# Performance work log

Hardware: AMD Instinct MI355X
Metric: run time of the kernel (lower is better)

The kernel has to match this reference:

```python
import jax, jax.numpy as jnp
import numpy as np

N, C = 4194304, 10
EPS = 1e-10
FOCAL_EPS = 1e-8
TEMP, THETA = 0.01, 0.1
NUM_TH = 21


def setup_inputs() -> dict:
    key = jax.random.key(0)
    k1, k2 = jax.random.split(key)
    logits = jax.random.normal(k1, (N, C), dtype=jnp.float32)
    probs = jax.nn.softmax(logits, axis=1)
    labels = jax.random.randint(k2, (N,), 0, C)
    y = jax.nn.one_hot(labels, C, dtype=jnp.float32)
    return {"probs": probs, "y": y}


def _soft_T(e):
    # sigmoid( (1/temp) * log( e*(1-theta) / clamp((1-e)*theta, eps) ) )
    num = e * (1.0 - THETA)
    den = jnp.maximum((1.0 - e) * THETA, EPS)
    frac = jnp.maximum(num / den, EPS)
    return jax.nn.sigmoid(jnp.log(frac) / TEMP)


def reference(probs, y):
    entmax = jnp.log(jnp.asarray(C, dtype=probs.dtype))
    predictions = jnp.argmax(probs, axis=1)             # [N]
    labels = jnp.argmax(y)                              # scalar (flattened argmax, as in torch code)

    # predictive uncertainty (type=0): entropy of probs per-sample
    unc = -jnp.sum(probs * jnp.log(jnp.maximum(probs, EPS)), axis=1)  # [N]

    th_list = jnp.linspace(0.0, 1.0, NUM_TH, dtype=probs.dtype)       # [21]
    umin, umax = jnp.min(unc), jnp.max(unc)
    unc_th = umin + th_list * (umax - umin)                           # [21]

    s = _soft_T(unc / entmax)                                         # [N]
    t = jnp.tanh(unc)                                                 # [N]
    w_cert = (1.0 - s) * (1.0 - t)   # weight when counted as 'certain'
    w_unc = s * t                    # weight when counted as 'uncertain'

    acc = (predictions == labels).astype(probs.dtype)                 # [N]
    inacc = 1.0 - acc

    le = (unc[None, :] <= unc_th[:, None]).astype(probs.dtype)        # [21, N]
    gt = 1.0 - le

    # one parallel masked-reduction pass over all 21 thresholds
    n_ac = le @ (acc * w_cert)
    n_au = gt @ (acc * w_unc)
    n_ic = le @ (inacc * w_cert)
    n_iu = gt @ (inacc * w_unc)

    avu = (n_ac + n_iu) / (n_ac + n_au + n_ic + n_iu + EPS)           # [21]

    # trapezoid rule over increasing th_list (direction = +1)
    dx = jnp.diff(th_list)
    auc_avu = jnp.sum((avu[1:] + avu[:-1]) * 0.5 * dx)

    # FocalLoss(gamma=1)
    logp = jnp.log(jnp.maximum(probs, FOCAL_EPS))
    ce_per = -jnp.sum(y * logp, axis=1)
    focal_per = -jnp.sum(y * logp * (1.0 - probs), axis=1)
    focal_loss = jnp.mean(focal_per)
    ce_loss = jnp.mean(ce_per)

    beta = 1.0
    savu_loss = -beta * jnp.log(jnp.maximum(auc_avu, EPS)) + focal_loss
    return (savu_loss, ce_loss)
```

## Files before the change

### kernel.cpp

```cpp
#include <hip/hip_runtime.h>

#define C 10
#define CHUNK_ROWS 128
#define CHUNK_FLOATS 1280

__device__ __forceinline__ float waveSum(float v) {
#pragma unroll
  for (int o = 32; o > 0; o >>= 1) v += __shfl_down(v, o, 64);
  return v;
}
__device__ __forceinline__ float waveMin(float v) {
#pragma unroll
  for (int o = 32; o > 0; o >>= 1) v = fminf(v, __shfl_down(v, o, 64));
  return v;
}
__device__ __forceinline__ float waveMax(float v) {
#pragma unroll
  for (int o = 32; o > 0; o >>= 1) v = fmaxf(v, __shfl_down(v, o, 64));
  return v;
}
__device__ __forceinline__ unsigned waveMaxU(unsigned v) {
#pragma unroll
  for (int o = 32; o > 0; o >>= 1) {
    unsigned w = (unsigned)__shfl_down((int)v, o, 64);
    v = v > w ? v : w;
  }
  return v;
}

#define GLD16(gp, lp)                                             \
  __builtin_amdgcn_global_load_lds(                               \
      (__attribute__((address_space(1))) void*)(gp),              \
      (__attribute__((address_space(3))) void*)(lp), 16, 0, 0)

__global__ __launch_bounds__(128, 2) void pass1(
    const float* __restrict__ probs, const float* __restrict__ y,
    float2* __restrict__ us2,
    unsigned* __restrict__ uminInvSlots, unsigned* __restrict__ umaxSlots,
    float* __restrict__ ceSlots, float* __restrict__ focalSlots,
    int nchunks) {
  __shared__ float lds[2 * 2 * 2 * CHUNK_FLOATS];
  __shared__ float red[8];
  const int tid = threadIdx.x;
  const int widx = tid >> 6, lane = tid & 63;
  float* const wbase = lds + widx * (4 * CHUNK_FLOATS);

  const int gw = blockIdx.x * 2 + widx;
  const int NW = gridDim.x * 2;

  int label0 = 0;
  {
    float m = y[0];
#pragma unroll
    for (int c = 1; c < C; ++c) {
      float v = y[c];
      if (v > m) { m = v; label0 = c; }
    }
  }

  auto issue = [&](int c, int b) {
    const size_t g = (size_t)c * CHUNK_FLOATS + (size_t)lane * 4;
    float* lp = wbase + b * (2 * CHUNK_FLOATS);
#pragma unroll
    for (int q = 0; q < 5; ++q)
      GLD16(probs + g + q * 256, lp + q * 256 + lane * 4);
#pragma unroll
    for (int q = 0; q < 5; ++q)
      GLD16(y + g + q * 256, lp + CHUNK_FLOATS + q * 256 + lane * 4);
  };

  float ceA = 0.f, foA = 0.f;
  float mnA = __uint_as_float(0x7f800000u), mxA = 0.f;

  if (gw < nchunks) issue(gw, 0);
  int b = 0;
  for (int c = gw; c < nchunks; c += NW, b ^= 1) {
    if (c + NW < nchunks) issue(c + NW, b ^ 1);

    const float4* pp = (const float4*)(wbase + b * (2 * CHUNK_FLOATS));
    const float4* yy = (const float4*)(wbase + b * (2 * CHUNK_FLOATS) + CHUNK_FLOATS);
    float P[20], Yv[20];
#pragma unroll
    for (int q = 0; q < 5; ++q) {
      float4 v = pp[lane * 5 + q];
      P[4 * q] = v.x; P[4 * q + 1] = v.y; P[4 * q + 2] = v.z; P[4 * q + 3] = v.w;
    }
#pragma unroll
    for (int q = 0; q < 5; ++q) {
      float4 v = yy[lane * 5 + q];
      Yv[4 * q] = v.x; Yv[4 * q + 1] = v.y; Yv[4 * q + 2] = v.z; Yv[4 * q + 3] = v.w;
    }

    int am0 = 0, am1 = 0;
    float m0 = P[0], m1 = P[10];
#pragma unroll
    for (int cc = 1; cc < C; ++cc) {
      if (P[cc] > m0) { m0 = P[cc]; am0 = cc; }
      if (P[10 + cc] > m1) { m1 = P[10 + cc]; am1 = cc; }
    }
    float u0 = 0.f, u1 = 0.f, pl0 = 0.f, pl1 = 0.f;
#pragma unroll
    for (int cc = 0; cc < C; ++cc) {
      u0 -= P[cc] * __logf(fmaxf(P[cc], 1e-10f));
      u1 -= P[10 + cc] * __logf(fmaxf(P[10 + cc], 1e-10f));
      pl0 = fmaf(Yv[cc], P[cc], pl0);
      pl1 = fmaf(Yv[10 + cc], P[10 + cc], pl1);
    }
    float ce0 = -__logf(fmaxf(pl0, 1e-8f)), ce1 = -__logf(fmaxf(pl1, 1e-8f));
    ceA += ce0 + ce1;
    foA += ce0 * (1.f - pl0) + ce1 * (1.f - pl1);
    mnA = fminf(mnA, fminf(u0, u1));
    mxA = fmaxf(mxA, fmaxf(u0, u1));

    unsigned s0 = __float_as_uint(u0) | ((am0 == label0) ? 0u : 0x80000000u);
    unsigned s1 = __float_as_uint(u1) | ((am1 == label0) ? 0u : 0x80000000u);
    us2[(size_t)c * 64 + lane] = make_float2(__uint_as_float(s0), __uint_as_float(s1));
  }

  float ce = waveSum(ceA), fo = waveSum(foA);
  float mn = waveMin(mnA), mx = waveMax(mxA);
  if (lane == 0) { red[widx] = ce; red[2 + widx] = fo; red[4 + widx] = mn; red[6 + widx] = mx; }
  __syncthreads();
  if (tid == 0) {
    float tce = red[0] + red[1];
    float tfo = red[2] + red[3];
    float tmn = fminf(red[4], red[5]);
    float tmx = fmaxf(red[6], red[7]);
    int slot = blockIdx.x & 63;
    atomicAdd(&ceSlots[slot], tce);
    atomicAdd(&focalSlots[slot], tfo);
    atomicMax(&uminInvSlots[slot], ~__float_as_uint(tmn));
    atomicMax(&umaxSlots[slot], __float_as_uint(tmx));
  }
}

__global__ __launch_bounds__(256, 4) void pass2(
    const float4* __restrict__ us4, int n4,
    const unsigned* __restrict__ uminInvSlots, const unsigned* __restrict__ umaxSlots,
    float* __restrict__ ghist) {
  __shared__ float hist[88 * 64];
  __shared__ float smm[2];
  const int tid = threadIdx.x, lane = tid & 63;
  for (int i = tid; i < 88 * 64; i += 256) hist[i] = 0.f;
  if (tid < 64) {
    unsigned mnInv = waveMaxU(uminInvSlots[tid]);
    unsigned mxb = waveMaxU(umaxSlots[tid]);
    if (tid == 0) { smm[0] = __uint_as_float(~mnInv); smm[1] = __uint_as_float(mxb); }
  }
  __syncthreads();
  const float umin = smm[0], delta = smm[1] - smm[0];
  float th[21];
#pragma unroll
  for (int k = 0; k < 21; ++k) th[k] = fmaf(0.05f * (float)k, delta, umin);

  const int stride = gridDim.x * 256;
  for (int i = blockIdx.x * 256 + tid; i < n4; i += stride) {
    float4 v = us4[i];
    float vv[4] = {v.x, v.y, v.z, v.w};
#pragma unroll
    for (int q = 0; q < 4; ++q) {
      unsigned b = __float_as_uint(vv[q]);
      int rb = (b >> 31) ? 44 : 0;
      float u = __uint_as_float(b & 0x7fffffffu);
      float e = u * 0.4342944819f;
      float lnum = __logf(e * 0.9f);
      float lden = __logf(fmaxf((1.f - e) * 0.1f, 1e-10f));
      float x = fmaxf(lnum - lden, -23.0258509f) * 100.f;
      float s = __builtin_amdgcn_rcpf(1.f + __expf(-x));
      float t = 1.f - 2.f * __builtin_amdgcn_rcpf(__expf(2.f * u) + 1.f);
      float wc = (1.f - s) * (1.f - t), wu = s * t;
      int j = 0;
#pragma unroll
      for (int k = 0; k < 21; ++k) j += (u > th[k]) ? 1 : 0;
      atomicAdd(&hist[(rb + j) * 64 + lane], wc);
      atomicAdd(&hist[(rb + 22 + j) * 64 + lane], wu);
    }
  }
  __syncthreads();
#pragma unroll
  for (int st = 32; st >= 1; st >>= 1) {
    for (int idx = tid; idx < 88 * st; idx += 256) {
      int r = idx / st, c = idx - r * st;
      hist[r * 64 + c] += hist[r * 64 + c + st];
    }
    __syncthreads();
  }
  int slot = blockIdx.x & 63;
  for (int r = tid; r < 88; r += 256)
    atomicAdd(&ghist[slot * 88 + r], hist[r * 64]);
}

__global__ __launch_bounds__(256) void pass3(
    const float* __restrict__ ghist,
    const float* __restrict__ ceSlots, const float* __restrict__ focalSlots,
    float* __restrict__ out, float invN) {
  __shared__ float hr[88];
  __shared__ float scf[2];
  int tid = threadIdx.x;
  if (tid < 88) {
    float s = 0.f;
    for (int q = 0; q < 64; ++q) s += ghist[q * 88 + tid];
    hr[tid] = s;
  }
  if (tid >= 128 && tid < 192) {
    int l = tid - 128;
    float ce = waveSum(ceSlots[l]);
    float fo = waveSum(focalSlots[l]);
    if (l == 0) { scf[0] = ce; scf[1] = fo; }
  }
  __syncthreads();
  if (tid == 0) {
    float H0[22], H1[22], H2[22], H3[22];
    float totAU = 0.f, totIU = 0.f;
    for (int j = 0; j < 22; ++j) {
      H0[j] = hr[j]; H1[j] = hr[22 + j]; H2[j] = hr[44 + j]; H3[j] = hr[66 + j];
      totAU += H1[j]; totIU += H3[j];
    }
    float n_ac = 0.f, n_ic = 0.f, n_au = totAU, n_iu = totIU;
    float auc = 0.f, prev = 0.f;
    for (int k = 0; k < 21; ++k) {
      n_ac += H0[k]; n_ic += H2[k];
      n_au -= H1[k]; n_iu -= H3[k];
      float avu = (n_ac + n_iu) / (n_ac + n_au + n_ic + n_iu + 1e-10f);
      if (k > 0) auc += (avu + prev) * 0.5f * 0.05f;
      prev = avu;
    }
    out[0] = -logf(fmaxf(auc, 1e-10f)) + scf[1] * invN;
    out[1] = scf[0] * invN;
  }
}

extern "C" void kernel_launch(void* const* d_in, const int* in_sizes, int n_in,
                              void* d_out, int out_size, void* d_ws, size_t ws_size,
                              hipStream_t stream) {
  const float* probs = (const float*)d_in[0];
  const float* y = (const float*)d_in[1];
  float* out = (float*)d_out;
  const int N = in_sizes[0] / C;

  float* wsf = (float*)d_ws;
  unsigned* uminInvSlots = (unsigned*)wsf;
  unsigned* umaxSlots = (unsigned*)(wsf + 64);
  float* ceSlots = wsf + 128;
  float* focalSlots = wsf + 192;
  float* ghist = wsf + 256;
  float* us = wsf + 5888;

  hipMemsetAsync(d_ws, 0, 5888 * sizeof(float), stream);

  const int nchunks = N / CHUNK_ROWS;
  pass1<<<1024, 128, 0, stream>>>(probs, y, (float2*)us, uminInvSlots, umaxSlots,
                                  ceSlots, focalSlots, nchunks);
  pass2<<<1024, 256, 0, stream>>>((const float4*)us, N / 4, uminInvSlots, umaxSlots,
                                  ghist);
  pass3<<<1, 256, 0, stream>>>(ghist, ceSlots, focalSlots, out, 1.0f / (float)N);
}
```

Baseline: 406.4 us.

## Load y directly to registers, compute focal terms per-element, widen pass1 blocks

The one-hot y tensor is now prefetched straight into registers in a coalesced layout instead of being staged through LDS, which halves LDS use per wave. The cross-entropy and focal terms are computed elementwise, as sum(y*log p) and sum(y*log p*(1-p)), instead of via the gathered label probability. Blocks grow to 4 waves, so the grid has twice as many waves, and the per-block shared reduction is replaced by per-wave atomics. This costs more log evaluations per element, more registers for the double-buffered y values, and more atomics.

After: 399.9 us. No clear change (-1.6%).

```diff
diff --git a/kernel.cpp b/kernel.cpp
--- a/kernel.cpp
+++ b/kernel.cpp
@@ -33,20 +33,19 @@
       (__attribute__((address_space(1))) void*)(gp),              \
       (__attribute__((address_space(3))) void*)(lp), 16, 0, 0)
 
-__global__ __launch_bounds__(128, 2) void pass1(
+__global__ __launch_bounds__(256, 4) void pass1(
     const float* __restrict__ probs, const float* __restrict__ y,
     float2* __restrict__ us2,
     unsigned* __restrict__ uminInvSlots, unsigned* __restrict__ umaxSlots,
     float* __restrict__ ceSlots, float* __restrict__ focalSlots,
     int nchunks) {
-  __shared__ float lds[2 * 2 * 2 * CHUNK_FLOATS];
-  __shared__ float red[8];
+  __shared__ float lds[4 * 2 * CHUNK_FLOATS];
   const int tid = threadIdx.x;
   const int widx = tid >> 6, lane = tid & 63;
-  float* const wbase = lds + widx * (4 * CHUNK_FLOATS);
-
-  const int gw = blockIdx.x * 2 + widx;
-  const int NW = gridDim.x * 2;
+  float* const wbuf = lds + widx * (2 * CHUNK_FLOATS);
+
+  const int gw = blockIdx.x * 4 + widx;
+  const int NW = gridDim.x * 4;
 
   int label0 = 0;
   {
@@ -58,39 +57,49 @@
     }
   }
 
-  auto issue = [&](int c, int b) {
-    const size_t g = (size_t)c * CHUNK_FLOATS + (size_t)lane * 4;
-    float* lp = wbase + b * (2 * CHUNK_FLOATS);
-#pragma unroll
-    for (int q = 0; q < 5; ++q)
-      GLD16(probs + g + q * 256, lp + q * 256 + lane * 4);
-#pragma unroll
-    for (int q = 0; q < 5; ++q)
-      GLD16(y + g + q * 256, lp + CHUNK_FLOATS + q * 256 + lane * 4);
+  const float4* y4 = (const float4*)y;
+
+  auto issueP = [&](int c, int b) {
+    const float* gp = probs + (size_t)c * CHUNK_FLOATS + (size_t)lane * 4;
+    float* lp = wbuf + b * CHUNK_FLOATS + lane * 4;
+#pragma unroll
+    for (int q = 0; q < 5; ++q) GLD16(gp + q * 256, lp + q * 256);
+  };
+  auto issueY = [&](int c, float4* Yr) {
+    const float4* gy = y4 + (size_t)c * 320 + lane;
+#pragma unroll
+    for (int q = 0; q < 5; ++q) Yr[q] = gy[q * 64];
   };
 
   float ceA = 0.f, foA = 0.f;
   float mnA = __uint_as_float(0x7f800000u), mxA = 0.f;
-
-  if (gw < nchunks) issue(gw, 0);
+  float4 Ycur[5], Ynxt[5];
+
+  if (gw < nchunks) { issueP(gw, 0); issueY(gw, Ycur); }
   int b = 0;
   for (int c = gw; c < nchunks; c += NW, b ^= 1) {
-    if (c + NW < nchunks) issue(c + NW, b ^ 1);
-
-    const float4* pp = (const float4*)(wbase + b * (2 * CHUNK_FLOATS));
-    const float4* yy = (const float4*)(wbase + b * (2 * CHUNK_FLOATS) + CHUNK_FLOATS);
-    float P[20], Yv[20];
+    if (c + NW < nchunks) { issueP(c + NW, b ^ 1); issueY(c + NW, Ynxt); }
+    const float4* buff4 = (const float4*)(wbuf + b * CHUNK_FLOATS);
+
 #pragma unroll
     for (int q = 0; q < 5; ++q) {
-      float4 v = pp[lane * 5 + q];
+      float4 pv = buff4[q * 64 + lane];
+      float4 yv = Ycur[q];
+      float lpx = __logf(fmaxf(pv.x, 1e-8f));
+      float lpy = __logf(fmaxf(pv.y, 1e-8f));
+      float lpz = __logf(fmaxf(pv.z, 1e-8f));
+      float lpw = __logf(fmaxf(pv.w, 1e-8f));
+      float tx = yv.x * lpx, ty = yv.y * lpy, tz = yv.z * lpz, tw = yv.w * lpw;
+      ceA -= tx + ty + tz + tw;
+      foA -= tx * (1.f - pv.x) + ty * (1.f - pv.y) + tz * (1.f - pv.z) + tw * (1.f - pv.w);
+    }
+
+    float P[20];
+#pragma unroll
+    for (int q = 0; q < 5; ++q) {
+      float4 v = buff4[lane * 5 + q];
       P[4 * q] = v.x; P[4 * q + 1] = v.y; P[4 * q + 2] = v.z; P[4 * q + 3] = v.w;
     }
-#pragma unroll
-    for (int q = 0; q < 5; ++q) {
-      float4 v = yy[lane * 5 + q];
-      Yv[4 * q] = v.x; Yv[4 * q + 1] = v.y; Yv[4 * q + 2] = v.z; Yv[4 * q + 3] = v.w;
-    }
-
     int am0 = 0, am1 = 0;
     float m0 = P[0], m1 = P[10];
 #pragma unroll
@@ -98,39 +107,31 @@
       if (P[cc] > m0) { m0 = P[cc]; am0 = cc; }
       if (P[10 + cc] > m1) { m1 = P[10 + cc]; am1 = cc; }
     }
-    float u0 = 0.f, u1 = 0.f, pl0 = 0.f, pl1 = 0.f;
+    float u0 = 0.f, u1 = 0.f;
 #pragma unroll
     for (int cc = 0; cc < C; ++cc) {
       u0 -= P[cc] * __logf(fmaxf(P[cc], 1e-10f));
       u1 -= P[10 + cc] * __logf(fmaxf(P[10 + cc], 1e-10f));
-      pl0 = fmaf(Yv[cc], P[cc], pl0);
-      pl1 = fmaf(Yv[10 + cc], P[10 + cc], pl1);
-    }
-    float ce0 = -__logf(fmaxf(pl0, 1e-8f)), ce1 = -__logf(fmaxf(pl1, 1e-8f));
-    ceA += ce0 + ce1;
-    foA += ce0 * (1.f - pl0) + ce1 * (1.f - pl1);
+    }
     mnA = fminf(mnA, fminf(u0, u1));
     mxA = fmaxf(mxA, fmaxf(u0, u1));
 
     unsigned s0 = __float_as_uint(u0) | ((am0 == label0) ? 0u : 0x80000000u);
     unsigned s1 = __float_as_uint(u1) | ((am1 == label0) ? 0u : 0x80000000u);
     us2[(size_t)c * 64 + lane] = make_float2(__uint_as_float(s0), __uint_as_float(s1));
+
+#pragma unroll
+    for (int q = 0; q < 5; ++q) Ycur[q] = Ynxt[q];
   }
 
   float ce = waveSum(ceA), fo = waveSum(foA);
   float mn = waveMin(mnA), mx = waveMax(mxA);
-  if (lane == 0) { red[widx] = ce; red[2 + widx] = fo; red[4 + widx] = mn; red[6 + widx] = mx; }
-  __syncthreads();
-  if (tid == 0) {
-    float tce = red[0] + red[1];
-    float tfo = red[2] + red[3];
-    float tmn = fminf(red[4], red[5]);
-    float tmx = fmaxf(red[6], red[7]);
-    int slot = blockIdx.x & 63;
-    atomicAdd(&ceSlots[slot], tce);
-    atomicAdd(&focalSlots[slot], tfo);
-    atomicMax(&uminInvSlots[slot], ~__float_as_uint(tmn));
-    atomicMax(&umaxSlots[slot], __float_as_uint(tmx));
+  if (lane == 0) {
+    int slot = gw & 63;
+    atomicAdd(&ceSlots[slot], ce);
+    atomicAdd(&focalSlots[slot], fo);
+    atomicMax(&uminInvSlots[slot], ~__float_as_uint(mn));
+    atomicMax(&umaxSlots[slot], __float_as_uint(mx));
   }
 }
 
@@ -249,7 +250,7 @@
   hipMemsetAsync(d_ws, 0, 5888 * sizeof(float), stream);
 
   const int nchunks = N / CHUNK_ROWS;
-  pass1<<<1024, 128, 0, stream>>>(probs, y, (float2*)us, uminInvSlots, umaxSlots,
+  pass1<<<1024, 256, 0, stream>>>(probs, y, (float2*)us, uminInvSlots, umaxSlots,
                                   ceSlots, focalSlots, nchunks);
   pass2<<<1024, 256, 0, stream>>>((const float4*)us, N / 4, uminInvSlots, umaxSlots,
                                   ghist);
```
